# Optimization experiments

Measured on AMD Instinct MI355X. Metric: run time of the kernel, lower is better.

The kernel has to match this reference:

```python
import jax, jax.numpy as jnp
import numpy as np
import math

WS = 12          # window side
N = WS * WS      # tokens per window = 144
C = 384          # channels
H = 12           # heads
NW = 4           # num windows per image (mask dim)
BW = 512         # total windows (num_windows * B)


def _rel_tables():
    # log-spaced continuous relative coords table, shape ((2*WS-1)^2, 2)
    r = np.arange(-(WS - 1), WS, dtype=np.float32)
    rc = np.stack(np.meshgrid(r, r, indexing='ij'), axis=-1)  # (2W-1, 2W-1, 2)
    rc = rc / (WS - 1) * WS
    table = np.sign(rc) * np.log2(np.abs(rc) + 1.0) / np.log2(8.0)
    # pairwise relative position index, shape (N, N)
    c = np.stack(np.meshgrid(np.arange(WS), np.arange(WS), indexing='ij')).reshape(2, -1)
    rel = (c[:, :, None] - c[:, None, :]).transpose(1, 2, 0)  # (N, N, 2)
    rel[..., 0] += WS - 1
    rel[..., 1] += WS - 1
    rel[..., 0] *= 2 * WS - 1
    idx = rel.sum(-1)
    return jnp.asarray(table.reshape(-1, 2)), jnp.asarray(idx)


def setup_inputs() -> dict:
    key = jax.random.key(0)
    ks = jax.random.split(key, 8)
    return {
        'x': jax.random.normal(ks[0], (BW, N, C), jnp.float32),
        'mask': jax.random.normal(ks[1], (NW, N, N), jnp.float32),
        'qkv_w': jax.random.normal(ks[2], (3 * C, C), jnp.float32) * 0.02,
        'qkv_b': jnp.zeros((3 * C,), jnp.float32),
        'logit_scale': jnp.log(10.0) * jnp.ones((H, 1, 1), jnp.float32),
        'cpb_w1': jax.random.normal(ks[3], (512, 2), jnp.float32) * 0.02,
        'cpb_b1': jnp.zeros((512,), jnp.float32),
        'cpb_w2': jax.random.normal(ks[4], (H, 512), jnp.float32) * 0.02,
        'proj_w': jax.random.normal(ks[5], (C, C), jnp.float32) * 0.02,
        'proj_b': jnp.zeros((C,), jnp.float32),
    }


def _l2norm(t):
    # F.normalize(dim=-1): divide by L2 norm clamped at 1e-12
    n = jnp.sqrt(jnp.sum(t * t, axis=-1, keepdims=True))
    return t / jnp.maximum(n, 1e-12)


def reference(x, mask, qkv_w, qkv_b, logit_scale, cpb_w1, cpb_b1, cpb_w2, proj_w, proj_b):
    table, idx = _rel_tables()
    B_, Nn, Cc = x.shape
    hd = Cc // H
    qkv = (x @ qkv_w.T + qkv_b).reshape(B_, Nn, 3, H, hd).transpose(2, 0, 3, 1, 4)
    q, k, v = qkv[0], qkv[1], qkv[2]  # each (B_, H, N, hd)

    # cosine attention with learned, clamped logit scale
    attn = jnp.einsum('bhnd,bhmd->bhnm', _l2norm(q), _l2norm(k))
    scale = jnp.exp(jnp.minimum(logit_scale, math.log(1.0 / 0.01)))  # (H,1,1)
    attn = attn * scale[None]

    # CPB-MLP relative position bias
    bias_tab = jax.nn.relu(table @ cpb_w1.T + cpb_b1) @ cpb_w2.T  # (529, H)
    bias = bias_tab[idx.reshape(-1)].reshape(Nn, Nn, H).transpose(2, 0, 1)
    attn = attn + 16.0 * jax.nn.sigmoid(bias)[None]

    # shifted-window mask add, then softmax
    num_win = mask.shape[0]
    attn = attn.reshape(B_ // num_win, num_win, H, Nn, Nn) + mask[None, :, None]
    attn = jax.nn.softmax(attn.reshape(B_, H, Nn, Nn), axis=-1)

    out = jnp.einsum('bhnm,bhmd->bnhd', attn, v).reshape(B_, Nn, Cc)
    return out @ proj_w.T + proj_b
```

## Files before the change

### kernel.cpp

```cpp
#include <hip/hip_runtime.h>
#include <hip/hip_fp16.h>


typedef _Float16 half8 __attribute__((ext_vector_type(8)));
typedef _Float16 half4v __attribute__((ext_vector_type(4)));
typedef float floatx4 __attribute__((ext_vector_type(4)));

#define BW 512
#define NTOK 144
#define CDIM 384
#define NH 12
#define HD 32
#define MROWS (BW * NTOK)
#define QKVN (3 * CDIM)

__device__ inline void llds16(const void* g, void* l) {
    __builtin_amdgcn_global_load_lds((const __attribute__((address_space(1))) void*)g,
                                     (__attribute__((address_space(3))) void*)l, 16, 0, 0);
}

__global__ __launch_bounds__(256) void cast_f2h(const float* __restrict__ s,
                                                _Float16* __restrict__ d, int n8) {
    int i = blockIdx.x * 256 + threadIdx.x;
    if (i >= n8) return;
    const float4* s4 = (const float4*)s;
    float4 a = s4[2 * i], b = s4[2 * i + 1];
    half8 h;
    h[0] = (_Float16)a.x; h[1] = (_Float16)a.y; h[2] = (_Float16)a.z; h[3] = (_Float16)a.w;
    h[4] = (_Float16)b.x; h[5] = (_Float16)b.y; h[6] = (_Float16)b.z; h[7] = (_Float16)b.w;
    ((half8*)d)[i] = h;
}

__global__ __launch_bounds__(256) void cast_weights(const float* __restrict__ w_qkv,
                                                    _Float16* __restrict__ qh,
                                                    const float* __restrict__ w_proj,
                                                    _Float16* __restrict__ ph) {
    const int nq = QKVN * CDIM / 8;
    const int np = CDIM * CDIM / 8;
    int i = blockIdx.x * 256 + threadIdx.x;
    const float4* s4; half8* d8; int j;
    if (i < nq) { s4 = (const float4*)w_qkv; d8 = (half8*)qh; j = i; }
    else if (i < nq + np) { s4 = (const float4*)w_proj; d8 = (half8*)ph; j = i - nq; }
    else return;
    float4 a = s4[2 * j], b = s4[2 * j + 1];
    half8 h;
    h[0] = (_Float16)a.x; h[1] = (_Float16)a.y; h[2] = (_Float16)a.z; h[3] = (_Float16)a.w;
    h[4] = (_Float16)b.x; h[5] = (_Float16)b.y; h[6] = (_Float16)b.z; h[7] = (_Float16)b.w;
    d8[j] = h;
}

__global__ void cpb_table(const float* __restrict__ w1, const float* __restrict__ b1,
                          const float* __restrict__ w2, float* __restrict__ tab) {
    int t = threadIdx.x;
    if (t >= 529) return;
    float u0 = (float)((t / 23) - 11) * (12.0f / 11.0f);
    float u1 = (float)((t % 23) - 11) * (12.0f / 11.0f);
    float x0 = copysignf(log2f(fabsf(u0) + 1.0f) * (1.0f / 3.0f), u0);
    float x1 = copysignf(log2f(fabsf(u1) + 1.0f) * (1.0f / 3.0f), u1);
    float acc[12] = {};
    for (int j = 0; j < 512; j++) {
        float hj = fmaf(x0, w1[2 * j], fmaf(x1, w1[2 * j + 1], b1[j]));
        hj = fmaxf(hj, 0.0f);
#pragma unroll
        for (int q = 0; q < 12; q++) acc[q] += hj * w2[q * 512 + j];
    }
    for (int q = 0; q < 12; q++) tab[t * 12 + q] = acc[q];
}

__global__ __launch_bounds__(256) void build_cm(const float* __restrict__ mask,
                                                const float* __restrict__ tab,
                                                float* __restrict__ CM) {
    int e = blockIdx.x * 256 + threadIdx.x;
    if (e >= 4 * NH * NTOK * NTOK) return;
    int j = e % NTOK; int r1 = e / NTOK;
    int i = r1 % NTOK; int r2 = r1 / NTOK;
    int h = r2 % NH;   int m = r2 / NH;
    int rt = ((i / 12) - (j / 12) + 11) * 23 + ((i % 12) - (j % 12) + 11);
    float bv = tab[rt * 12 + h];
    CM[e] = mask[m * (NTOK * NTOK) + i * NTOK + j] + 16.0f / (1.0f + __expf(-bv));
}

template <typename OutT>
__global__ __launch_bounds__(512) void gemm_bt(const _Float16* __restrict__ A,
                                               const _Float16* __restrict__ B,
                                               const float* __restrict__ bias,
                                               OutT* __restrict__ C, int M, int N, int K) {
    __shared__ __align__(16) _Float16 As[2][256 * 32];
    __shared__ __align__(16) _Float16 Bs[2][128 * 32];
    const int t = threadIdx.x;
    const int wv = t >> 6, l = t & 63;
    const int wm = wv >> 1, wn = wv & 1;
    const int lr = l & 15, lk = l >> 4;

    const int ntn = N >> 7;
    const int t8 = gridDim.x >> 3;
    const int tile = (blockIdx.x & 7) * t8 + (blockIdx.x >> 3);
    const long m0 = (long)(tile / ntn) * 256, n0 = (long)(tile % ntn) * 128;

    const int srow = t >> 2, scol = (t & 3) * 8;
    const _Float16* ag = A + (m0 + srow) * (long)K + scol;
    const _Float16* bg = B + (n0 + srow) * (long)K + scol;

    floatx4 acc[4][4] = {};
    const int nk = K >> 5;
    int cur = 0;

    llds16(ag, &As[0][t * 8]);
    llds16(ag + 128 * (long)K, &As[0][t * 8 + 4096]);
    llds16(bg, &Bs[0][t * 8]);
    ag += 32; bg += 32;
    __syncthreads();

    for (int it = 0; it < nk - 1; ++it) {
        llds16(ag, &As[cur ^ 1][t * 8]);
        llds16(ag + 128 * (long)K, &As[cur ^ 1][t * 8 + 4096]);
        llds16(bg, &Bs[cur ^ 1][t * 8]);
        ag += 32; bg += 32;

        half8 af[4], bf[4];
#pragma unroll
        for (int fi = 0; fi < 4; fi++)
            af[fi] = *(const half8*)&As[cur][(wm * 64 + fi * 16 + lr) * 32 + lk * 8];
#pragma unroll
        for (int fj = 0; fj < 4; fj++)
            bf[fj] = *(const half8*)&Bs[cur][(wn * 64 + fj * 16 + lr) * 32 + lk * 8];
#pragma unroll
        for (int fi = 0; fi < 4; fi++)
#pragma unroll
            for (int fj = 0; fj < 4; fj++)
                acc[fi][fj] = __builtin_amdgcn_mfma_f32_16x16x32_f16(af[fi], bf[fj], acc[fi][fj], 0, 0, 0);

        __syncthreads();
        cur ^= 1;
    }

    {
        half8 af[4], bf[4];
#pragma unroll
        for (int fi = 0; fi < 4; fi++)
            af[fi] = *(const half8*)&As[cur][(wm * 64 + fi * 16 + lr) * 32 + lk * 8];
#pragma unroll
        for (int fj = 0; fj < 4; fj++)
            bf[fj] = *(const half8*)&Bs[cur][(wn * 64 + fj * 16 + lr) * 32 + lk * 8];
#pragma unroll
        for (int fi = 0; fi < 4; fi++)
#pragma unroll
            for (int fj = 0; fj < 4; fj++)
                acc[fi][fj] = __builtin_amdgcn_mfma_f32_16x16x32_f16(af[fi], bf[fj], acc[fi][fj], 0, 0, 0);
    }

#pragma unroll
    for (int fi = 0; fi < 4; fi++) {
        const long row = m0 + wm * 64 + fi * 16 + lk * 4;
#pragma unroll
        for (int fj = 0; fj < 4; fj++) {
            const long col = n0 + wn * 64 + fj * 16 + lr;
            const float bv = bias[col];
#pragma unroll
            for (int r = 0; r < 4; r++) {
                float v = acc[fi][fj][r] + bv;
                C[(row + r) * (long)N + col] = (OutT)v;
            }
        }
    }
}

__global__ __launch_bounds__(576) void attn_win(const _Float16* __restrict__ qkv,
                                                const float* __restrict__ CM,
                                                const float* __restrict__ lscale,
                                                _Float16* __restrict__ O) {
    __shared__ __align__(16) _Float16 Kn[NTOK * HD];
    __shared__ __align__(16) _Float16 Vt[HD * NTOK];

    const int bid = blockIdx.x;
    const int w = bid / NH, h = bid % NH;
    const int t = threadIdx.x;
    const int wv = t >> 6, l = t & 63;
    const int lr = l & 15, lk = l >> 4;

    const float sc = expf(fminf(lscale[h], 4.6051701859880914f));

    {
        const int row = t >> 2, part = t & 3;
        const size_t base = (size_t)(w * NTOK + row) * QKVN + h * HD + part * 8;
        half8 kv = *(const half8*)(qkv + base + CDIM);
        float ss = 0.f;
#pragma unroll
        for (int j = 0; j < 8; j++) { float f = (float)kv[j]; ss += f * f; }
        ss += __shfl_xor(ss, 1); ss += __shfl_xor(ss, 2);
        float inv = 1.0f / fmaxf(sqrtf(ss), 1e-12f);
        half8 kn;
#pragma unroll
        for (int j = 0; j < 8; j++) kn[j] = (_Float16)((float)kv[j] * inv);
        *(half8*)&Kn[row * HD + part * 8] = kn;

        half8 vv = *(const half8*)(qkv + base + 2 * CDIM);
#pragma unroll
        for (int j = 0; j < 8; j++) Vt[(part * 8 + j) * NTOK + row] = vv[j];
    }

    half8 aq;
    {
        const size_t qb = (size_t)(w * NTOK + wv * 16 + lr) * QKVN + h * HD + lk * 8;
        half8 q = *(const half8*)(qkv + qb);
        float ss = 0.f;
#pragma unroll
        for (int j = 0; j < 8; j++) { float f = (float)q[j]; ss += f * f; }
        ss += __shfl_xor(ss, 16); ss += __shfl_xor(ss, 32);
        float inv = sc / fmaxf(sqrtf(ss), 1e-12f);
#pragma unroll
        for (int j = 0; j < 8; j++) aq[j] = (_Float16)((float)q[j] * inv);
    }
    __syncthreads();

    floatx4 s[9];
#pragma unroll
    for (int cj = 0; cj < 9; cj++) {
        half8 bk = *(const half8*)&Kn[(cj * 16 + lr) * HD + lk * 8];
        floatx4 z = {};
        s[cj] = __builtin_amdgcn_mfma_f32_16x16x32_f16(bk, aq, z, 0, 0, 0);
    }
    const float* cmb = CM + (size_t)((w & 3) * NH + h) * (NTOK * NTOK)
                     + (size_t)(wv * 16 + lr) * NTOK + lk * 4;
#pragma unroll
    for (int cj = 0; cj < 9; cj++) {
        float4 c4 = *(const float4*)(cmb + cj * 16);
        s[cj][0] += c4.x; s[cj][1] += c4.y; s[cj][2] += c4.z; s[cj][3] += c4.w;
    }

    float m = s[0][0];
#pragma unroll
    for (int cj = 0; cj < 9; cj++)
#pragma unroll
        for (int r = 0; r < 4; r++) m = fmaxf(m, s[cj][r]);
    m = fmaxf(m, __shfl_xor(m, 16)); m = fmaxf(m, __shfl_xor(m, 32));
    float sum = 0.f;
#pragma unroll
    for (int cj = 0; cj < 9; cj++)
#pragma unroll
        for (int r = 0; r < 4; r++) { s[cj][r] = __expf(s[cj][r] - m); sum += s[cj][r]; }
    sum += __shfl_xor(sum, 16); sum += __shfl_xor(sum, 32);
    const float inv = 1.0f / sum;

    half4v pa[9];
#pragma unroll
    for (int cj = 0; cj < 9; cj++) {
        pa[cj][0] = (_Float16)s[cj][0]; pa[cj][1] = (_Float16)s[cj][1];
        pa[cj][2] = (_Float16)s[cj][2]; pa[cj][3] = (_Float16)s[cj][3];
    }

    floatx4 o0 = {}, o1 = {};
#pragma unroll
    for (int cj = 0; cj < 9; cj++) {
        half4v v0 = *(const half4v*)&Vt[lr * NTOK + cj * 16 + lk * 4];
        half4v v1 = *(const half4v*)&Vt[(16 + lr) * NTOK + cj * 16 + lk * 4];
        o0 = __builtin_amdgcn_mfma_f32_16x16x16f16(v0, pa[cj], o0, 0, 0, 0);
        o1 = __builtin_amdgcn_mfma_f32_16x16x16f16(v1, pa[cj], o1, 0, 0, 0);
    }

    const size_t ob = (size_t)(w * NTOK + wv * 16 + lr) * CDIM + h * HD + lk * 4;
    half4v r0, r1;
#pragma unroll
    for (int r = 0; r < 4; r++) {
        r0[r] = (_Float16)(o0[r] * inv);
        r1[r] = (_Float16)(o1[r] * inv);
    }
    *(half4v*)&O[ob] = r0;
    *(half4v*)&O[ob + 16] = r1;
}

extern "C" void kernel_launch(void* const* d_in, const int* in_sizes, int n_in,
                              void* d_out, int out_size, void* d_ws, size_t ws_size,
                              hipStream_t stream) {
    const float* x     = (const float*)d_in[0];
    const float* mask  = (const float*)d_in[1];
    const float* qkv_w = (const float*)d_in[2];
    const float* qkv_b = (const float*)d_in[3];
    const float* lsc   = (const float*)d_in[4];
    const float* cw1   = (const float*)d_in[5];
    const float* cb1   = (const float*)d_in[6];
    const float* cw2   = (const float*)d_in[7];
    const float* pw    = (const float*)d_in[8];
    const float* pb    = (const float*)d_in[9];
    (void)in_sizes; (void)n_in; (void)out_size; (void)ws_size;

    char* ws = (char*)d_ws;
    float*    tab  = (float*)(ws);
    float*    CM   = (float*)(ws + 25600);
    _Float16* qw_h = (_Float16*)(ws + 4006912);
    _Float16* pw_h = (_Float16*)(ws + 4891648);
    _Float16* x_h  = (_Float16*)(ws + 5186560);
    _Float16* qkvh = (_Float16*)(ws + 61809664);
    _Float16* o_h  = x_h;

    cast_f2h<<<(MROWS * CDIM / 8) / 256, 256, 0, stream>>>(x, x_h, MROWS * CDIM / 8);
    cast_weights<<<(QKVN * CDIM / 8 + CDIM * CDIM / 8 + 255) / 256, 256, 0, stream>>>(
        qkv_w, qw_h, pw, pw_h);
    cpb_table<<<1, 576, 0, stream>>>(cw1, cb1, cw2, tab);
    build_cm<<<(4 * NH * NTOK * NTOK + 255) / 256, 256, 0, stream>>>(mask, tab, CM);

    gemm_bt<_Float16><<<(QKVN / 128) * (MROWS / 256), 512, 0, stream>>>(
        x_h, qw_h, qkv_b, qkvh, MROWS, QKVN, CDIM);

    attn_win<<<BW * NH, 576, 0, stream>>>(qkvh, CM, lsc, o_h);

    gemm_bt<float><<<(CDIM / 128) * (MROWS / 256), 512, 0, stream>>>(
        o_h, pw_h, pb, (float*)d_out, MROWS, CDIM, CDIM);
}
```

Measured before the change: 510.0 us.

## Triple-buffer GEMM LDS stages with a single barrier per k-step

The fp16 MFMA GEMM moves from two to three LDS buffers and prefetches two k-tiles ahead. Each iteration now has one partial s_waitcnt vmcnt(3) plus one barrier, replacing the full __syncthreads after compute, so global-to-LDS loads overlap more with MFMA work. Row offsets are also hoisted out of the fragment loads. The cost is a larger LDS footprint per block (72KB instead of 48KB), which can lower how many blocks fit on a CU.

```diff
diff --git a/kernel.cpp b/kernel.cpp
--- a/kernel.cpp
+++ b/kernel.cpp
@@ -85,8 +85,8 @@
                                                const _Float16* __restrict__ B,
                                                const float* __restrict__ bias,
                                                OutT* __restrict__ C, int M, int N, int K) {
-    __shared__ __align__(16) _Float16 As[2][256 * 32];
-    __shared__ __align__(16) _Float16 Bs[2][128 * 32];
+    __shared__ __align__(16) _Float16 As[3][256 * 32];
+    __shared__ __align__(16) _Float16 Bs[3][128 * 32];
     const int t = threadIdx.x;
     const int wv = t >> 6, l = t & 63;
     const int wm = wv >> 1, wn = wv & 1;
@@ -103,45 +103,58 @@
 
     floatx4 acc[4][4] = {};
     const int nk = K >> 5;
-    int cur = 0;
+    const int aoff = wm * 64 + lr, boff = wn * 64 + lr;
 
     llds16(ag, &As[0][t * 8]);
     llds16(ag + 128 * (long)K, &As[0][t * 8 + 4096]);
     llds16(bg, &Bs[0][t * 8]);
     ag += 32; bg += 32;
-    __syncthreads();
-
+    llds16(ag, &As[1][t * 8]);
+    llds16(ag + 128 * (long)K, &As[1][t * 8 + 4096]);
+    llds16(bg, &Bs[1][t * 8]);
+    ag += 32; bg += 32;
+
+    int cur = 0, nx2 = 2;
     for (int it = 0; it < nk - 1; ++it) {
-        llds16(ag, &As[cur ^ 1][t * 8]);
-        llds16(ag + 128 * (long)K, &As[cur ^ 1][t * 8 + 4096]);
-        llds16(bg, &Bs[cur ^ 1][t * 8]);
-        ag += 32; bg += 32;
+        asm volatile("s_waitcnt vmcnt(3)" ::: "memory");
+        __builtin_amdgcn_s_barrier();
+        __builtin_amdgcn_sched_barrier(0);
+
+        if (it + 2 < nk) {
+            llds16(ag, &As[nx2][t * 8]);
+            llds16(ag + 128 * (long)K, &As[nx2][t * 8 + 4096]);
+            llds16(bg, &Bs[nx2][t * 8]);
+            ag += 32; bg += 32;
+        }
 
         half8 af[4], bf[4];
 #pragma unroll
         for (int fi = 0; fi < 4; fi++)
-            af[fi] = *(const half8*)&As[cur][(wm * 64 + fi * 16 + lr) * 32 + lk * 8];
+            af[fi] = *(const half8*)&As[cur][(aoff + fi * 16) * 32 + lk * 8];
 #pragma unroll
         for (int fj = 0; fj < 4; fj++)
-            bf[fj] = *(const half8*)&Bs[cur][(wn * 64 + fj * 16 + lr) * 32 + lk * 8];
+            bf[fj] = *(const half8*)&Bs[cur][(boff + fj * 16) * 32 + lk * 8];
 #pragma unroll
         for (int fi = 0; fi < 4; fi++)
 #pragma unroll
             for (int fj = 0; fj < 4; fj++)
                 acc[fi][fj] = __builtin_amdgcn_mfma_f32_16x16x32_f16(af[fi], bf[fj], acc[fi][fj], 0, 0, 0);
 
-        __syncthreads();
-        cur ^= 1;
+        cur = (cur == 2) ? 0 : cur + 1;
+        nx2 = (nx2 == 2) ? 0 : nx2 + 1;
     }
 
     {
+        asm volatile("s_waitcnt vmcnt(0)" ::: "memory");
+        __builtin_amdgcn_s_barrier();
+        __builtin_amdgcn_sched_barrier(0);
         half8 af[4], bf[4];
 #pragma unroll
         for (int fi = 0; fi < 4; fi++)
-            af[fi] = *(const half8*)&As[cur][(wm * 64 + fi * 16 + lr) * 32 + lk * 8];
+            af[fi] = *(const half8*)&As[cur][(aoff + fi * 16) * 32 + lk * 8];
 #pragma unroll
         for (int fj = 0; fj < 4; fj++)
-            bf[fj] = *(const half8*)&Bs[cur][(wn * 64 + fj * 16 + lr) * 32 + lk * 8];
+            bf[fj] = *(const half8*)&Bs[cur][(boff + fj * 16) * 32 + lk * 8];
 #pragma unroll
         for (int fi = 0; fi < 4; fi++)
 #pragma unroll
```

After: 514.0 us. No clear change (+0.8%).
